# Performance work log

Hardware: AMD Instinct MI355X
Metric: run time of the kernel (lower is better)

## Reference

```python
import jax, jax.numpy as jnp
import numpy as np

NUM_HEADS = 1
HIDDEN = 256
HEAD_DIM = HIDDEN // NUM_HEADS
SCALE = HEAD_DIM ** -0.5


def _rotate_pairwise(x):
    # (... , d) -> rotate adjacent pairs: (x0,x1,x2,x3,..) -> (-x1,x0,-x3,x2,..)
    shape = x.shape
    x = x.reshape(*shape[:-1], -1, 2)
    x = jnp.stack([-x[..., 1], x[..., 0]], axis=-1)
    return x.reshape(shape)


def setup_inputs() -> dict:
    key = jax.random.key(0)
    ks = jax.random.split(key, 12)
    B, PB, QS, KS = 1, 1, 4096, 16448
    KV_IN = 64
    d = {
        'query': jax.random.normal(ks[0], (B, PB, QS, HIDDEN), jnp.float32),
        'key': jax.random.normal(ks[1], (B, PB, KS, KV_IN), jnp.float32),
        'value': jax.random.normal(ks[2], (B, PB, KS, KV_IN), jnp.float32),
        'rope_cos': jax.random.normal(ks[3], (QS, HEAD_DIM), jnp.float32),
        'rope_sin': jax.random.normal(ks[4], (QS, HEAD_DIM), jnp.float32),
        'wq': jax.random.normal(ks[5], (HIDDEN, HIDDEN), jnp.float32) * (HIDDEN ** -0.5),
        'bq': jnp.zeros((HIDDEN,), jnp.float32),
        'wk': jax.random.normal(ks[6], (KV_IN, HIDDEN), jnp.float32) * (KV_IN ** -0.5),
        'bk': jnp.zeros((HIDDEN,), jnp.float32),
        'wv': jax.random.normal(ks[7], (KV_IN, HIDDEN), jnp.float32) * (KV_IN ** -0.5),
        'bv': jnp.zeros((HIDDEN,), jnp.float32),
        'wo': jax.random.normal(ks[8], (HIDDEN, HIDDEN), jnp.float32) * (HIDDEN ** -0.5),
        'bo': jnp.zeros((HIDDEN,), jnp.float32),
        'num_k_exclude_rope': 64,
    }
    return d


def reference(query, key, value, rope_cos, rope_sin, wq, bq, wk, bk, wv, bv, wo, bo, num_k_exclude_rope):
    batch, pb, qs, _ = query.shape
    ks = key.shape[2]
    B = batch * pb
    # projections -> [B, H, S, hd]
    q = (query @ wq + bq).reshape(B, qs, NUM_HEADS, HEAD_DIM).transpose(0, 2, 1, 3)
    k = (key @ wk + bk).reshape(B, ks, NUM_HEADS, HEAD_DIM).transpose(0, 2, 1, 3)
    v = (value @ wv + bv).reshape(B, ks, NUM_HEADS, HEAD_DIM).transpose(0, 2, 1, 3)
    cos = rope_cos[None, None]  # [1,1,QS,hd]
    sin = rope_sin[None, None]
    # split off non-RoPE keys (object pointer tokens)
    n_rot = ks - num_k_exclude_rope
    k_rot, k_pass = k[:, :, :n_rot, :], k[:, :, n_rot:, :]
    q = q * cos + _rotate_pairwise(q) * sin
    if n_rot != qs:  # rope_k_repeat branch (static shapes)
        rep = n_rot // qs
        cos_k = jnp.repeat(cos, rep, axis=2)
        sin_k = jnp.repeat(sin, rep, axis=2)
    else:
        cos_k, sin_k = cos, sin
    k_emb = k_rot * cos_k + _rotate_pairwise(k_rot) * sin_k
    k = jnp.concatenate([k_emb, k_pass], axis=-2)
    attn = jax.nn.softmax(jnp.einsum('bhqd,bhkd->bhqk', q * SCALE, k), axis=-1)
    x = jnp.einsum('bhqk,bhkd->bhqd', attn, v)
    x = x.transpose(0, 2, 1, 3).reshape(batch, pb, qs, HIDDEN)
    return x @ wo + bo
```

## Files before the change

### kernel.cpp

```cpp
#include <hip/hip_runtime.h>
#include <hip/hip_bf16.h>

typedef __attribute__((ext_vector_type(4))) float floatx4;
typedef __attribute__((ext_vector_type(8))) short shortx8;
typedef __attribute__((ext_vector_type(8))) _Float16 halfx8;
typedef _Float16 half_t;

#define MFMA_BF16(A,B,C) __builtin_amdgcn_mfma_f32_16x16x32_bf16((A),(B),(C),0,0,0)
#define NEG_INF (-__builtin_inff())
#define GLOBAL_AS __attribute__((address_space(1)))
#define LDS_AS __attribute__((address_space(3)))

static __device__ __forceinline__ unsigned short f2b(float f) {
    union { float f; unsigned u; } v; v.f = f;
    unsigned r = v.u + 0x7FFFu + ((v.u >> 16) & 1u);
    return (unsigned short)(r >> 16);
}
static __device__ __forceinline__ unsigned pack_bf16(float lo, float hi) {
    return (unsigned)f2b(lo) | ((unsigned)f2b(hi) << 16);
}
static __device__ __forceinline__ unsigned pack_half(float lo, float hi) {
    union { half_t h[2]; unsigned u; } p;
    p.h[0] = (half_t)lo; p.h[1] = (half_t)hi;
    return p.u;
}
static __device__ __forceinline__ float EXP2F(float x) { return __builtin_amdgcn_exp2f(x); }

#define NSPLIT 8
#define NSPLIT_C 16
#define NTILES 257

__global__ __launch_bounds__(256) void wtrans_kernel(
    const float* __restrict__ wq, const float* __restrict__ wk,
    const float* __restrict__ wv, const float* __restrict__ wo,
    unsigned short* __restrict__ wqt, unsigned short* __restrict__ wkt,
    unsigned short* __restrict__ wvt, unsigned short* __restrict__ wot)
{
    __shared__ unsigned short tb[64 * 68];
    const int bid = blockIdx.x, tid = threadIdx.x;
    const float* src; unsigned short* dst; int K0, N0, Kfull;
    if (bid < 16)      { src = wq; dst = wqt; Kfull = 256; K0 = (bid >> 2) * 64; N0 = (bid & 3) * 64; }
    else if (bid < 20) { src = wk; dst = wkt; Kfull = 64;  K0 = 0; N0 = (bid - 16) * 64; }
    else if (bid < 24) { src = wv; dst = wvt; Kfull = 64;  K0 = 0; N0 = (bid - 20) * 64; }
    else { int t2 = bid - 24; src = wo; dst = wot; Kfull = 256; K0 = (t2 >> 2) * 64; N0 = (t2 & 3) * 64; }

    {
        const int r = tid >> 2, c0 = (tid & 3) * 16;
        const float* p = src + (K0 + r) * 256 + N0 + c0;
        #pragma unroll
        for (int j = 0; j < 16; j += 4) {
            floatx4 f = *(const floatx4*)(p + j);
            tb[r * 68 + c0 + j + 0] = f2b(f[0]);
            tb[r * 68 + c0 + j + 1] = f2b(f[1]);
            tb[r * 68 + c0 + j + 2] = f2b(f[2]);
            tb[r * 68 + c0 + j + 3] = f2b(f[3]);
        }
    }
    __syncthreads();
    {
        const int n = tid >> 2, k0 = (tid & 3) * 16;
        shortx8 v0, v1;
        #pragma unroll
        for (int j = 0; j < 8; j++) {
            v0[j] = tb[(k0 + j) * 68 + n];
            v1[j] = tb[(k0 + 8 + j) * 68 + n];
        }
        unsigned short* q = dst + (N0 + n) * Kfull + K0 + k0;
        *(shortx8*)q = v0;
        *(shortx8*)(q + 8) = v1;
    }
}

__global__ __launch_bounds__(256) void proj_kernel(
    const float* __restrict__ query, const float* __restrict__ key,
    const float* __restrict__ value,
    const unsigned short* __restrict__ wqt, const float* __restrict__ bq,
    const unsigned short* __restrict__ wkt, const float* __restrict__ bk,
    const unsigned short* __restrict__ wvt, const float* __restrict__ bv,
    const float* __restrict__ cosb, const float* __restrict__ sinb,
    const int* __restrict__ nkx,
    unsigned short* __restrict__ qr, unsigned short* __restrict__ krw,
    unsigned short* __restrict__ vtg)
{
    __shared__ unsigned short tbuf[256 * 72];
    const int tid = threadIdx.x;
    const int wave = tid >> 6, lane = tid & 63;
    const int c = lane & 15, quad = lane >> 4;
    const int bx = blockIdx.x;

    if (bx < 64) {
        const int m0 = bx * 64;
        shortx8 aA[8];
        {
            const int mrow = m0 + wave * 16 + c;
            #pragma unroll
            for (int ks = 0; ks < 8; ks++) {
                const float* p = query + mrow * 256 + ks * 32 + quad * 8;
                floatx4 f0 = *(const floatx4*)p;
                floatx4 f1 = *(const floatx4*)(p + 4);
                shortx8 a;
                #pragma unroll
                for (int j = 0; j < 4; j++) { a[j] = (short)f2b(f0[j]); a[j + 4] = (short)f2b(f1[j]); }
                aA[ks] = a;
            }
        }
        floatx4 acc[16];
        #pragma unroll
        for (int nt = 0; nt < 16; nt++) { acc[nt][0]=0.f; acc[nt][1]=0.f; acc[nt][2]=0.f; acc[nt][3]=0.f; }
        #pragma unroll
        for (int nt = 0; nt < 16; nt++) {
            #pragma unroll
            for (int ks = 0; ks < 8; ks++) {
                shortx8 b = *(const shortx8*)(wqt + (nt * 16 + c) * 256 + ks * 32 + quad * 8);
                acc[nt] = MFMA_BF16(aA[ks], b, acc[nt]);
            }
        }
        const float sc = 0.09016844005556021f;
        #pragma unroll
        for (int nt = 0; nt < 16; nt++) {
            const int col = nt * 16 + c;
            float vals[4];
            #pragma unroll
            for (int r = 0; r < 4; r++) {
                const int row = m0 + wave * 16 + quad * 4 + r;
                float v = acc[nt][r] + bq[col];
                float partner = __shfl_xor(v, 1);
                float cv = cosb[row * 256 + col];
                float sn = sinb[row * 256 + col];
                float rot = (col & 1) ? partner : -partner;
                vals[r] = (v * cv + rot * sn) * sc;
            }
            #pragma unroll
            for (int r2 = 0; r2 < 4; r2 += 2) {
                float a = vals[r2], b = vals[r2 + 1];
                float ax = __shfl_xor(a, 1), bx2 = __shfl_xor(b, 1);
                float lo = (c & 1) ? bx2 : a;
                float hi = (c & 1) ? b : ax;
                int row = m0 + wave * 16 + quad * 4 + r2 + (c & 1);
                *(unsigned*)(qr + row * 256 + nt * 16 + (c & ~1)) = pack_bf16(lo, hi);
            }
        }
        return;
    }

    const int isv = (bx >= 321);
    const int m0 = (isv ? (bx - 321) : (bx - 64)) * 64;
    const float* src = isv ? value : key;
    const unsigned short* wt = isv ? wvt : wkt;
    const float* bias = isv ? bv : bk;

    shortx8 aA[2];
    {
        const int mrow = m0 + wave * 16 + c;
        #pragma unroll
        for (int ks = 0; ks < 2; ks++) {
            const float* p = src + mrow * 64 + ks * 32 + quad * 8;
            floatx4 f0 = *(const floatx4*)p;
            floatx4 f1 = *(const floatx4*)(p + 4);
            shortx8 a;
            #pragma unroll
            for (int j = 0; j < 4; j++) { a[j] = (short)f2b(f0[j]); a[j + 4] = (short)f2b(f1[j]); }
            aA[ks] = a;
        }
    }
    floatx4 acc[16];
    #pragma unroll
    for (int nt = 0; nt < 16; nt++) { acc[nt][0]=0.f; acc[nt][1]=0.f; acc[nt][2]=0.f; acc[nt][3]=0.f; }
    #pragma unroll
    for (int nt = 0; nt < 16; nt++) {
        #pragma unroll
        for (int ks = 0; ks < 2; ks++) {
            shortx8 b = *(const shortx8*)(wt + (nt * 16 + c) * 64 + ks * 32 + quad * 8);
            acc[nt] = MFMA_BF16(aA[ks], b, acc[nt]);
        }
    }
    if (!isv) {
        const int n_rot = 16448 - nkx[0];
        int rep = n_rot / 4096; if (rep < 1) rep = 1;
        int rc4[4];
        #pragma unroll
        for (int r = 0; r < 4; r++) {
            int row = m0 + wave * 16 + quad * 4 + r;
            rc4[r] = row / rep;
        }
        #pragma unroll
        for (int nt = 0; nt < 16; nt++) {
            const int col = nt * 16 + c;
            float vals[4];
            #pragma unroll
            for (int r = 0; r < 4; r++) {
                const int row = m0 + wave * 16 + quad * 4 + r;
                float v = acc[nt][r] + bias[col];
                float partner = __shfl_xor(v, 1);
                float outv = v;
                if (row < n_rot) {
                    float cv = cosb[rc4[r] * 256 + col];
                    float sn = sinb[rc4[r] * 256 + col];
                    float rot = (col & 1) ? partner : -partner;
                    outv = v * cv + rot * sn;
                }
                vals[r] = outv;
            }
            #pragma unroll
            for (int r2 = 0; r2 < 4; r2 += 2) {
                float a = vals[r2], b = vals[r2 + 1];
                float ax = __shfl_xor(a, 1), bx2 = __shfl_xor(b, 1);
                float lo = (c & 1) ? bx2 : a;
                float hi = (c & 1) ? b : ax;
                int row = m0 + wave * 16 + quad * 4 + r2 + (c & 1);
                *(unsigned*)(krw + row * 256 + nt * 16 + (c & ~1)) = pack_bf16(lo, hi);
            }
        }
    } else {
        #pragma unroll
        for (int nt = 0; nt < 16; nt++) {
            const int col = nt * 16 + c;
            #pragma unroll
            for (int r = 0; r < 4; r++) {
                const int rl = wave * 16 + quad * 4 + r;
                tbuf[col * 72 + rl] = f2b(acc[nt][r] + bias[col]);
            }
        }
        __syncthreads();
        #pragma unroll
        for (int i = 0; i < 8; i++) {
            int G = i * 256 + tid;
            int n = G >> 3, g = G & 7;
            *(floatx4*)(vtg + n * 16448 + m0 + g * 8) = *(const floatx4*)(tbuf + n * 72 + g * 8);
        }
    }
}

__global__ __launch_bounds__(512, 2) void flash_kernel(
    const unsigned short* __restrict__ qr, const unsigned short* __restrict__ kr,
    const unsigned short* __restrict__ vt, half_t* __restrict__ Opart,
    float* __restrict__ Lpart)
{
    __shared__ unsigned short smem[75776];
    const int tid = threadIdx.x;
    const int wave = tid >> 6, lane = tid & 63;
    const int c = lane & 15, quad = lane >> 4;
    const int cx = c & 7;
    const int qg = wave & 3, kvh = wave >> 2;
    const int qrow0 = blockIdx.x * 128 + qg * 32;
    const int s = blockIdx.y;
    const int t0 = (s * NTILES) / NSPLIT, t1 = ((s + 1) * NTILES) / NSPLIT;
    unsigned short* pw = smem + 65536 + wave * 1280;

    shortx8 aQ[2][8];
    #pragma unroll
    for (int u = 0; u < 2; u++)
        #pragma unroll
        for (int ks = 0; ks < 8; ks++)
            aQ[u][ks] = *(const shortx8*)(qr + (qrow0 + u * 16 + c) * 256 + ks * 32 + quad * 8);

    floatx4 o[2][16];
    #pragma unroll
    for (int u = 0; u < 2; u++)
        #pragma unroll
        for (int nt = 0; nt < 16; nt++) { o[u][nt][0]=0.f; o[u][nt][1]=0.f; o[u][nt][2]=0.f; o[u][nt][3]=0.f; }
    float l_i[2] = { 0.f, 0.f };

    auto stage = [&](int t, int buf) {
        const int kv0 = t * 64;
        unsigned short* kb = smem + buf * 16384;
        unsigned short* vb = smem + 32768 + buf * 16384;
        #pragma unroll
        for (int i = 0; i < 4; i++) {
            int L = i * 512 + tid;
            int kv = L >> 5, p = L & 31;
            int g = (p & 24) | ((p & 7) ^ (kv & 7));
            __builtin_amdgcn_global_load_lds(
                (const GLOBAL_AS void*)(const void*)(kr + (kv0 + kv) * 256 + g * 8),
                (LDS_AS void*)(void*)(kb + (i * 512 + wave * 64) * 8), 16, 0, 0);
        }
        #pragma unroll
        for (int i = 0; i < 4; i++) {
            int L = i * 512 + tid;
            int d = L >> 3, p = L & 7;
            int g = p ^ (d & 7);
            __builtin_amdgcn_global_load_lds(
                (const GLOBAL_AS void*)(const void*)(vt + d * 16448 + kv0 + g * 8),
                (LDS_AS void*)(void*)(vb + (i * 512 + wave * 64) * 8), 16, 0, 0);
        }
    };

    stage(t0, 0);
    int cur = 0;
    const int pv_p = (kvh * 4 + quad) ^ cx;
    for (int t = t0; t < t1; t++) {
        __syncthreads();
        if (t + 1 < t1) stage(t + 1, cur ^ 1);
        const unsigned short* kb = smem + cur * 16384;
        const unsigned short* vb = smem + 32768 + cur * 16384;

        floatx4 sv[2][2];
        #pragma unroll
        for (int u = 0; u < 2; u++)
            #pragma unroll
            for (int nt = 0; nt < 2; nt++) { sv[u][nt][0]=0.f; sv[u][nt][1]=0.f; sv[u][nt][2]=0.f; sv[u][nt][3]=0.f; }
        #pragma unroll
        for (int nt = 0; nt < 2; nt++) {
            const unsigned short* krow = kb + (kvh * 32 + nt * 16 + c) * 256;
            #pragma unroll
            for (int ks = 0; ks < 8; ks++) {
                int p = ((ks >> 1) * 8) | ((((ks & 1) << 2) + quad) ^ cx);
                shortx8 kfrag = *(const shortx8*)(krow + p * 8);
                sv[0][nt] = MFMA_BF16(kfrag, aQ[0][ks], sv[0][nt]);
                sv[1][nt] = MFMA_BF16(kfrag, aQ[1][ks], sv[1][nt]);
            }
        }
        #pragma unroll
        for (int u = 0; u < 2; u++) {
            float rs = 0.f;
            #pragma unroll
            for (int nt = 0; nt < 2; nt++)
                #pragma unroll
                for (int r = 0; r < 4; r++) {
                    float pv = EXP2F(sv[u][nt][r]);
                    sv[u][nt][r] = pv;
                    rs += pv;
                }
            l_i[u] += rs;
        }
        #pragma unroll
        for (int u = 0; u < 2; u++)
            #pragma unroll
            for (int nt = 0; nt < 2; nt++)
                #pragma unroll
                for (int r2 = 0; r2 < 4; r2 += 2)
                    *(unsigned*)(pw + (u * 16 + c) * 40 + nt * 16 + quad * 4 + r2) =
                        pack_bf16(sv[u][nt][r2], sv[u][nt][r2 + 1]);
        shortx8 aP[2];
        #pragma unroll
        for (int u = 0; u < 2; u++)
            aP[u] = *(const shortx8*)(pw + (u * 16 + c) * 40 + quad * 8);
        #pragma unroll
        for (int nt = 0; nt < 16; nt++) {
            const unsigned short* vrow = vb + (nt * 16 + c) * 64;
            shortx8 b0 = *(const shortx8*)(vrow + pv_p * 8);
            o[0][nt] = MFMA_BF16(aP[0], b0, o[0][nt]);
            o[1][nt] = MFMA_BF16(aP[1], b0, o[1][nt]);
        }
        cur ^= 1;
    }
    const int sEff = s * 2 + kvh;
    half_t* Ob = Opart + (size_t)sEff * (4096 * 256);
    #pragma unroll
    for (int u = 0; u < 2; u++) {
        l_i[u] += __shfl_xor(l_i[u], 16);
        l_i[u] += __shfl_xor(l_i[u], 32);
    }
    float inv[2] = { 1.0f / l_i[0], 1.0f / l_i[1] };
    #pragma unroll
    for (int u = 0; u < 2; u++) {
        float ar[4];
        #pragma unroll
        for (int r = 0; r < 4; r++) ar[r] = __shfl(inv[u], quad * 4 + r);
        #pragma unroll
        for (int nt = 0; nt < 16; nt++) {
            o[u][nt][0] *= ar[0]; o[u][nt][1] *= ar[1];
            o[u][nt][2] *= ar[2]; o[u][nt][3] *= ar[3];
        }
    }
    #pragma unroll
    for (int u = 0; u < 2; u++)
        #pragma unroll
        for (int nt = 0; nt < 16; nt++)
            #pragma unroll
            for (int r2 = 0; r2 < 4; r2 += 2) {
                float a = o[u][nt][r2], b = o[u][nt][r2 + 1];
                float ax = __shfl_xor(a, 1), bx2 = __shfl_xor(b, 1);
                float lo = (c & 1) ? bx2 : a;
                float hi = (c & 1) ? b : ax;
                int row = qrow0 + u * 16 + quad * 4 + r2 + (c & 1);
                *(unsigned*)(Ob + row * 256 + nt * 16 + (c & ~1)) = pack_half(lo, hi);
            }
    if (quad == 0) {
        #pragma unroll
        for (int u = 0; u < 2; u++)
            Lpart[sEff * 4096 + qrow0 + u * 16 + c] = l_i[u];
    }
}

__global__ __launch_bounds__(256) void combine_kernel(
    const half_t* __restrict__ Opart, const float* __restrict__ Lpart,
    unsigned short* __restrict__ xb)
{
    int idx = blockIdx.x * 256 + threadIdx.x;
    int row = idx >> 5;
    int d0 = (idx & 31) * 8;
    float wn[NSPLIT_C], den = 0.f;
    #pragma unroll
    for (int sp = 0; sp < NSPLIT_C; sp++) { wn[sp] = Lpart[sp * 4096 + row]; den += wn[sp]; }
    float inv = 1.0f / den;
    #pragma unroll
    for (int sp = 0; sp < NSPLIT_C; sp++) wn[sp] *= inv;
    float acc[8];
    #pragma unroll
    for (int j = 0; j < 8; j++) acc[j] = 0.f;
    #pragma unroll
    for (int sp = 0; sp < NSPLIT_C; sp++) {
        halfx8 hv = *(const halfx8*)(Opart + (size_t)sp * (4096 * 256) + row * 256 + d0);
        #pragma unroll
        for (int j = 0; j < 8; j++) acc[j] += wn[sp] * (float)hv[j];
    }
    shortx8 xv;
    #pragma unroll
    for (int j = 0; j < 8; j++) xv[j] = (short)f2b(acc[j]);
    *(shortx8*)(xb + row * 256 + d0) = xv;
}

__global__ __launch_bounds__(256) void oproj_kernel(
    const unsigned short* __restrict__ xb, const unsigned short* __restrict__ wot,
    const float* __restrict__ bo, float* __restrict__ outp)
{
    const int tid = threadIdx.x;
    const int wave = tid >> 6, lane = tid & 63;
    const int c = lane & 15, quad = lane >> 4;
    const int m0 = blockIdx.x * 64;
    const int n0 = blockIdx.y * 64;

    shortx8 aX[8];
    #pragma unroll
    for (int ks = 0; ks < 8; ks++)
        aX[ks] = *(const shortx8*)(xb + (m0 + wave * 16 + c) * 256 + ks * 32 + quad * 8);
    floatx4 acc[4];
    #pragma unroll
    for (int nt = 0; nt < 4; nt++) { acc[nt][0]=0.f; acc[nt][1]=0.f; acc[nt][2]=0.f; acc[nt][3]=0.f; }
    #pragma unroll
    for (int nt = 0; nt < 4; nt++) {
        #pragma unroll
        for (int ks = 0; ks < 8; ks++) {
            shortx8 b = *(const shortx8*)(wot + (n0 + nt * 16 + c) * 256 + ks * 32 + quad * 8);
            acc[nt] = MFMA_BF16(aX[ks], b, acc[nt]);
        }
    }
    #pragma unroll
    for (int nt = 0; nt < 4; nt++) {
        const int col = n0 + nt * 16 + c;
        #pragma unroll
        for (int r = 0; r < 4; r++) {
            const int row = m0 + wave * 16 + quad * 4 + r;
            outp[row * 256 + col] = acc[nt][r] + bo[col];
        }
    }
}

extern "C" void kernel_launch(void* const* d_in, const int* in_sizes, int n_in,
                              void* d_out, int out_size, void* d_ws, size_t ws_size,
                              hipStream_t stream) {
    const float* query = (const float*)d_in[0];
    const float* key   = (const float*)d_in[1];
    const float* value = (const float*)d_in[2];
    const float* cosb  = (const float*)d_in[3];
    const float* sinb  = (const float*)d_in[4];
    const float* wq    = (const float*)d_in[5];
    const float* bq    = (const float*)d_in[6];
    const float* wk    = (const float*)d_in[7];
    const float* bk    = (const float*)d_in[8];
    const float* wv    = (const float*)d_in[9];
    const float* bv    = (const float*)d_in[10];
    const float* wo    = (const float*)d_in[11];
    const float* bo    = (const float*)d_in[12];
    const int*   nk    = (const int*)d_in[13];

    char* ws = (char*)d_ws;
    unsigned short* wqt = (unsigned short*)(ws + 0);
    unsigned short* wkt = (unsigned short*)(ws + 131072);
    unsigned short* wvt = (unsigned short*)(ws + 163840);
    unsigned short* wot = (unsigned short*)(ws + 196608);
    unsigned short* qr  = (unsigned short*)(ws + 327680);
    unsigned short* xb  = (unsigned short*)(ws + 327680);
    unsigned short* krw = (unsigned short*)(ws + 2424832);
    unsigned short* vtg = (unsigned short*)(ws + 10846208);
    half_t* Opart = (half_t*)(ws + 19267584);
    float* Lpart = (float*)(ws + 52822016);
    float* outp  = (float*)d_out;

    wtrans_kernel<<<dim3(40), dim3(256), 0, stream>>>(wq, wk, wv, wo, wqt, wkt, wvt, wot);
    proj_kernel<<<dim3(578), dim3(256), 0, stream>>>(
        query, key, value, wqt, bq, wkt, bk, wvt, bv, cosb, sinb, nk, qr, krw, vtg);
    flash_kernel<<<dim3(32, NSPLIT), dim3(512), 0, stream>>>(qr, krw, vtg, Opart, Lpart);
    combine_kernel<<<dim3(512), dim3(256), 0, stream>>>(Opart, Lpart, xb);
    oproj_kernel<<<dim3(64, 4), dim3(256), 0, stream>>>(xb, wot, bo, outp);
}
```

Measured before the change: 231.7 us.

## Fuse combine into output projection, flatten flash grid, use hardware bf16 pack

Merges the split-KV combine and output projection into one kernel that reduces partial outputs into LDS and runs the MFMA projection from there. This removes a launch and the bf16 round trip through global memory. The flash kernel grid becomes 1D with split index in the low bits, so blocks sharing the same KV range and query rows sit closer in launch order. The P-matrix bf16 packing uses the v_cvt_pk_bf16_f32 instruction instead of manual rounding. The fused kernel launches only 256 blocks, which may reduce parallelism in the combine stage.

Result: faster. 225.5 us (-2.7%).

```diff
diff --git a/kernel.cpp b/kernel.cpp
--- a/kernel.cpp
+++ b/kernel.cpp
@@ -7,7 +7,6 @@
 typedef _Float16 half_t;
 
 #define MFMA_BF16(A,B,C) __builtin_amdgcn_mfma_f32_16x16x32_bf16((A),(B),(C),0,0,0)
-#define NEG_INF (-__builtin_inff())
 #define GLOBAL_AS __attribute__((address_space(1)))
 #define LDS_AS __attribute__((address_space(3)))
 
@@ -23,6 +22,11 @@
     union { half_t h[2]; unsigned u; } p;
     p.h[0] = (half_t)lo; p.h[1] = (half_t)hi;
     return p.u;
+}
+static __device__ __forceinline__ unsigned cvtpk_bf16(float lo, float hi) {
+    unsigned r;
+    asm("v_cvt_pk_bf16_f32 %0, %1, %2" : "=v"(r) : "v"(lo), "v"(hi));
+    return r;
 }
 static __device__ __forceinline__ float EXP2F(float x) { return __builtin_amdgcn_exp2f(x); }
 
@@ -242,8 +246,9 @@
     const int c = lane & 15, quad = lane >> 4;
     const int cx = c & 7;
     const int qg = wave & 3, kvh = wave >> 2;
-    const int qrow0 = blockIdx.x * 128 + qg * 32;
-    const int s = blockIdx.y;
+    const int s = blockIdx.x & 7;
+    const int xb = blockIdx.x >> 3;
+    const int qrow0 = xb * 128 + qg * 32;
     const int t0 = (s * NTILES) / NSPLIT, t1 = ((s + 1) * NTILES) / NSPLIT;
     unsigned short* pw = smem + 65536 + wave * 1280;
 
@@ -330,7 +335,7 @@
                 #pragma unroll
                 for (int r2 = 0; r2 < 4; r2 += 2)
                     *(unsigned*)(pw + (u * 16 + c) * 40 + nt * 16 + quad * 4 + r2) =
-                        pack_bf16(sv[u][nt][r2], sv[u][nt][r2 + 1]);
+                        cvtpk_bf16(sv[u][nt][r2], sv[u][nt][r2 + 1]);
         shortx8 aP[2];
         #pragma unroll
         for (int u = 0; u < 2; u++)
@@ -383,65 +388,67 @@
     }
 }
 
-__global__ __launch_bounds__(256) void combine_kernel(
+__global__ __launch_bounds__(256) void combine_oproj_kernel(
     const half_t* __restrict__ Opart, const float* __restrict__ Lpart,
-    unsigned short* __restrict__ xb)
+    const unsigned short* __restrict__ wot, const float* __restrict__ bo,
+    float* __restrict__ outp)
 {
-    int idx = blockIdx.x * 256 + threadIdx.x;
-    int row = idx >> 5;
-    int d0 = (idx & 31) * 8;
-    float wn[NSPLIT_C], den = 0.f;
-    #pragma unroll
-    for (int sp = 0; sp < NSPLIT_C; sp++) { wn[sp] = Lpart[sp * 4096 + row]; den += wn[sp]; }
-    float inv = 1.0f / den;
-    #pragma unroll
-    for (int sp = 0; sp < NSPLIT_C; sp++) wn[sp] *= inv;
-    float acc[8];
-    #pragma unroll
-    for (int j = 0; j < 8; j++) acc[j] = 0.f;
-    #pragma unroll
-    for (int sp = 0; sp < NSPLIT_C; sp++) {
-        halfx8 hv = *(const halfx8*)(Opart + (size_t)sp * (4096 * 256) + row * 256 + d0);
-        #pragma unroll
-        for (int j = 0; j < 8; j++) acc[j] += wn[sp] * (float)hv[j];
-    }
-    shortx8 xv;
-    #pragma unroll
-    for (int j = 0; j < 8; j++) xv[j] = (short)f2b(acc[j]);
-    *(shortx8*)(xb + row * 256 + d0) = xv;
-}
-
-__global__ __launch_bounds__(256) void oproj_kernel(
-    const unsigned short* __restrict__ xb, const unsigned short* __restrict__ wot,
-    const float* __restrict__ bo, float* __restrict__ outp)
-{
+    __shared__ unsigned short xt[16 * 264];
     const int tid = threadIdx.x;
-    const int wave = tid >> 6, lane = tid & 63;
+    const int m0 = blockIdx.x * 16;
+
+    {
+        const int d0 = (tid & 31) * 8;
+        #pragma unroll
+        for (int pass = 0; pass < 2; pass++) {
+            const int rl = pass * 8 + (tid >> 5);
+            const int row = m0 + rl;
+            float wn[NSPLIT_C], den = 0.f;
+            #pragma unroll
+            for (int sp = 0; sp < NSPLIT_C; sp++) { wn[sp] = Lpart[sp * 4096 + row]; den += wn[sp]; }
+            float inv = 1.0f / den;
+            float acc[8];
+            #pragma unroll
+            for (int j = 0; j < 8; j++) acc[j] = 0.f;
+            #pragma unroll
+            for (int sp = 0; sp < NSPLIT_C; sp++) {
+                halfx8 hv = *(const halfx8*)(Opart + (size_t)sp * (4096 * 256) + row * 256 + d0);
+                float w = wn[sp] * inv;
+                #pragma unroll
+                for (int j = 0; j < 8; j++) acc[j] += w * (float)hv[j];
+            }
+            shortx8 xv;
+            #pragma unroll
+            for (int j = 0; j < 8; j++) xv[j] = (short)f2b(acc[j]);
+            *(shortx8*)(xt + rl * 264 + d0) = xv;
+        }
+    }
+    __syncthreads();
+
+    const int lane = tid & 63, wave = tid >> 6;
     const int c = lane & 15, quad = lane >> 4;
-    const int m0 = blockIdx.x * 64;
-    const int n0 = blockIdx.y * 64;
-
     shortx8 aX[8];
     #pragma unroll
     for (int ks = 0; ks < 8; ks++)
-        aX[ks] = *(const shortx8*)(xb + (m0 + wave * 16 + c) * 256 + ks * 32 + quad * 8);
+        aX[ks] = *(const shortx8*)(xt + c * 264 + ks * 32 + quad * 8);
     floatx4 acc[4];
     #pragma unroll
     for (int nt = 0; nt < 4; nt++) { acc[nt][0]=0.f; acc[nt][1]=0.f; acc[nt][2]=0.f; acc[nt][3]=0.f; }
     #pragma unroll
     for (int nt = 0; nt < 4; nt++) {
+        const int n = (wave * 4 + nt) * 16;
         #pragma unroll
         for (int ks = 0; ks < 8; ks++) {
-            shortx8 b = *(const shortx8*)(wot + (n0 + nt * 16 + c) * 256 + ks * 32 + quad * 8);
+            shortx8 b = *(const shortx8*)(wot + (n + c) * 256 + ks * 32 + quad * 8);
             acc[nt] = MFMA_BF16(aX[ks], b, acc[nt]);
         }
     }
     #pragma unroll
     for (int nt = 0; nt < 4; nt++) {
-        const int col = n0 + nt * 16 + c;
+        const int col = (wave * 4 + nt) * 16 + c;
         #pragma unroll
         for (int r = 0; r < 4; r++) {
-            const int row = m0 + wave * 16 + quad * 4 + r;
+            const int row = m0 + quad * 4 + r;
             outp[row * 256 + col] = acc[nt][r] + bo[col];
         }
     }
@@ -471,7 +478,6 @@
     unsigned short* wvt = (unsigned short*)(ws + 163840);
     unsigned short* wot = (unsigned short*)(ws + 196608);
     unsigned short* qr  = (unsigned short*)(ws + 327680);
-    unsigned short* xb  = (unsigned short*)(ws + 327680);
     unsigned short* krw = (unsigned short*)(ws + 2424832);
     unsigned short* vtg = (unsigned short*)(ws + 10846208);
     half_t* Opart = (half_t*)(ws + 19267584);
@@ -481,7 +487,6 @@
     wtrans_kernel<<<dim3(40), dim3(256), 0, stream>>>(wq, wk, wv, wo, wqt, wkt, wvt, wot);
     proj_kernel<<<dim3(578), dim3(256), 0, stream>>>(
         query, key, value, wqt, bq, wkt, bk, wvt, bv, cosb, sinb, nk, qr, krw, vtg);
-    flash_kernel<<<dim3(32, NSPLIT), dim3(512), 0, stream>>>(qr, krw, vtg, Opart, Lpart);
-    combine_kernel<<<dim3(512), dim3(256), 0, stream>>>(Opart, Lpart, xb);
-    oproj_kernel<<<dim3(64, 4), dim3(256), 0, stream>>>(xb, wot, bo, outp);
-}
+    flash_kernel<<<dim3(256), dim3(512), 0, stream>>>(qr, krw, vtg, Opart, Lpart);
+    combine_oproj_kernel<<<dim3(256), dim3(256), 0, stream>>>(Opart, Lpart, wot, bo, outp);
+}
```
